# Performance work log

Measured on AMD Instinct MI355X. Metric: run time of the kernel, lower is better.

## Reference

```python
import jax, jax.numpy as jnp
from jax import lax
import numpy as np

B, C, H, W = 16, 64, 256, 256
K = 7


def setup_inputs() -> dict:
    key = jax.random.key(0)
    kx, kk = jax.random.split(key)
    x = jax.random.normal(kx, (B, C, H, W), dtype=jnp.float32)
    kernel = jax.random.normal(kk, (K, K), dtype=jnp.float32)
    return {"x": x, "kernel": kernel}


def reference(x, kernel):
    # Depthwise conv: every (b, ch) slice convolved with the SAME [K,K] kernel.
    # scipy-style true convolution => flip the kernel, 'same' padding.
    c = x.shape[1]
    kflip = jnp.flip(kernel, axis=(0, 1))
    w = jnp.tile(kflip[None, None], (c, 1, 1, 1))  # [C,1,K,K]
    y = lax.conv_general_dilated(
        x, w,
        window_strides=(1, 1),
        padding='SAME',
        feature_group_count=c,
        dimension_numbers=('NCHW', 'OIHW', 'NCHW'),
    )
    # mish(y) = y * tanh(softplus(y))
    return y * jnp.tanh(jax.nn.softplus(y))
```

## Files before the change

kernel.cpp:

```cpp
#include <hip/hip_runtime.h>


#define HW 256
#define PITCH 88
#define LROWS 70
#define NSTG 1400
#define TPB 8

typedef _Float16 f16x8 __attribute__((ext_vector_type(8)));
typedef float    f32x4 __attribute__((ext_vector_type(4)));
typedef __fp16   h2    __attribute__((ext_vector_type(2)));
union U32H2 { unsigned u; h2 h; };
union BFU   { uint4 u; f16x8 h; };

__device__ __forceinline__ float mish_f(float y) {
    float t = __expf(y);
    float u = 1.0f + t;
    float d = __fmaf_rn(u, u, 1.0f);
    return y * (1.0f - __fdividef(2.0f, d));
}

__global__ __launch_bounds__(256)
__attribute__((amdgpu_waves_per_eu(3, 5)))
void dwconv7_mish_mfma3(const float* __restrict__ x,
                        const float* __restrict__ kern,
                        float* __restrict__ out) {
    __shared__ __align__(16) _Float16 lds_in[2][LROWS * PITCH];
    __shared__ __align__(16) unsigned lds_B[7 * 256];

    const int tid = threadIdx.x;
    const int bid = blockIdx.x;
    const int plane = bid >> 1;
    const int sbase = (bid & 1) << 3;

    const float* __restrict__ xp = x + (size_t)plane * (HW * HW);
    float* __restrict__ op = out + (size_t)plane * (HW * HW);

    float kf[49];
    #pragma unroll
    for (int i = 0; i < 49; ++i) {
        int p = i / 7, q = i - p * 7;
        kf[i] = __int_as_float(__builtin_amdgcn_readfirstlane(
                    __float_as_int(kern[(6 - p) * 7 + (6 - q)])));
    }

    {
        const int j  = tid >> 4;
        const int kw = tid & 15;
        #pragma unroll
        for (int p = 0; p < 7; ++p) {
            const int d0 = 2 * kw - j - 5;
            const int d1 = d0 + 1;
            float v0 = 0.f, v1 = 0.f;
            #pragma unroll
            for (int q = 0; q < 7; ++q) {
                v0 = (d0 == q) ? kf[p * 7 + q] : v0;
                v1 = (d1 == q) ? kf[p * 7 + q] : v1;
            }
            U32H2 u; u.h = __builtin_amdgcn_cvt_pkrtz(v0, v1);
            lds_B[p * 256 + tid] = u.u;
        }
    }

    int ro_[6], co_[6], lo_[6];
    #pragma unroll
    for (int it = 0; it < 6; ++it) {
        int idx = tid + it * 256;
        int r = idx / 20, g = idx - 20 * r;
        ro_[it] = r - 3;
        co_[it] = 4 * g - 8;
        lo_[it] = r * 22 + g;
    }

    {
        const int c0 = (sbase & 3) << 6, r0 = (sbase >> 2) << 6;
        #pragma unroll
        for (int it = 0; it < 6; ++it) {
            if (it < 5 || tid < NSTG - 1280) {
                int gr = r0 + ro_[it], gc = c0 + co_[it];
                float4 f = make_float4(0.f, 0.f, 0.f, 0.f);
                if ((unsigned)gr < (unsigned)HW && (unsigned)gc <= (unsigned)(HW - 4))
                    f = *(const float4*)(xp + (gr << 8) + gc);
                U32H2 a, b;
                a.h = __builtin_amdgcn_cvt_pkrtz(f.x, f.y);
                b.h = __builtin_amdgcn_cvt_pkrtz(f.z, f.w);
                ((uint2*)lds_in[0])[lo_[it]] = make_uint2(a.u, b.u);
            }
        }
    }
    __syncthreads();

    const int lane = tid & 63;
    const int w    = tid >> 6;
    const int lrow = lane & 15;
    const int lk   = lane >> 4;

    f16x8 bfrag[7];
    #pragma unroll
    for (int p = 0; p < 7; ++p) {
        BFU bu;
        bu.u = ((const uint4*)lds_B)[p * 64 + lrow * 4 + lk];
        bfrag[p] = bu.h;
    }

    float4 rf[6];

    #pragma unroll 1
    for (int t = 0; t < TPB; ++t) {
        const int s  = sbase + t;
        const int c0 = (s & 3) << 6, r0 = (s >> 2) << 6;

        if (t + 1 < TPB) {
            const int s2 = sbase + t + 1;
            const int c2 = (s2 & 3) << 6, r2 = (s2 >> 2) << 6;
            #pragma unroll
            for (int it = 0; it < 6; ++it) {
                if (it < 5 || tid < NSTG - 1280) {
                    int gr = r2 + ro_[it], gc = c2 + co_[it];
                    rf[it] = make_float4(0.f, 0.f, 0.f, 0.f);
                    if ((unsigned)gr < (unsigned)HW && (unsigned)gc <= (unsigned)(HW - 4))
                        rf[it] = *(const float4*)(xp + (gr << 8) + gc);
                }
            }
        }
        __builtin_amdgcn_sched_barrier(0);

        const _Float16* bufp = lds_in[t & 1];
        #pragma unroll
        for (int t4 = 0; t4 < 4; ++t4) {
            f32x4 acc = {0.f, 0.f, 0.f, 0.f};
            #pragma unroll
            for (int p = 0; p < 7; ++p) {
                f16x8 a = *(const f16x8*)(bufp +
                            (16 * w + lrow + p) * PITCH + 16 * t4 + 8 * lk);
                acc = __builtin_amdgcn_mfma_f32_16x16x32_f16(a, bfrag[p], acc,
                                                             0, 0, 0);
            }
            const int col   = c0 + 16 * t4 + lrow;
            const int rbase = r0 + 16 * w + 4 * lk;
            op[(rbase + 0) * HW + col] = mish_f(acc[0]);
            op[(rbase + 1) * HW + col] = mish_f(acc[1]);
            op[(rbase + 2) * HW + col] = mish_f(acc[2]);
            op[(rbase + 3) * HW + col] = mish_f(acc[3]);
        }
        __builtin_amdgcn_sched_barrier(0);

        if (t + 1 < TPB) {
            #pragma unroll
            for (int it = 0; it < 6; ++it) {
                if (it < 5 || tid < NSTG - 1280) {
                    U32H2 a, b;
                    a.h = __builtin_amdgcn_cvt_pkrtz(rf[it].x, rf[it].y);
                    b.h = __builtin_amdgcn_cvt_pkrtz(rf[it].z, rf[it].w);
                    ((uint2*)lds_in[(t + 1) & 1])[lo_[it]] = make_uint2(a.u, b.u);
                }
            }
        }
        __syncthreads();
    }
}

extern "C" void kernel_launch(void* const* d_in, const int* in_sizes, int n_in,
                              void* d_out, int out_size, void* d_ws, size_t ws_size,
                              hipStream_t stream) {
    const float* x = (const float*)d_in[0];
    const float* k = (const float*)d_in[1];
    float* out = (float*)d_out;

    dim3 grid(2 * 16 * 64, 1, 1);
    dim3 block(256);
    dwconv7_mish_mfma3<<<grid, block, 0, stream>>>(x, k, out);
}
```

Baseline: 132.6 us.

## Give each wavefront a private double-buffered halo tile to drop block barriers

Work moves from a block-shared 64x64 tile with a 70-row LDS halo to one in which each wavefront owns a 16x64 strip with its own 22-row double-buffered LDS region. A wave loads, converts and computes its own data, so the per-tile __syncthreads is removed and waves run independently. In exchange, the halo rows loaded per output row rise from about 70/64 to 22/16, which adds redundant global loads, and LDS per block grows. The waves_per_eu upper bound is also tightened.

```diff
diff --git a/kernel.cpp b/kernel.cpp
--- a/kernel.cpp
+++ b/kernel.cpp
@@ -3,9 +3,8 @@
 
 #define HW 256
 #define PITCH 88
-#define LROWS 70
-#define NSTG 1400
-#define TPB 8
+#define WROWS 22
+#define TPW 8
 
 typedef _Float16 f16x8 __attribute__((ext_vector_type(8)));
 typedef float    f32x4 __attribute__((ext_vector_type(4)));
@@ -21,17 +20,19 @@
 }
 
 __global__ __launch_bounds__(256)
-__attribute__((amdgpu_waves_per_eu(3, 5)))
-void dwconv7_mish_mfma3(const float* __restrict__ x,
+__attribute__((amdgpu_waves_per_eu(3, 4)))
+void dwconv7_mish_mfma4(const float* __restrict__ x,
                         const float* __restrict__ kern,
                         float* __restrict__ out) {
-    __shared__ __align__(16) _Float16 lds_in[2][LROWS * PITCH];
+    __shared__ __align__(16) _Float16 lds_in[4][2][WROWS * PITCH];
     __shared__ __align__(16) unsigned lds_B[7 * 256];
 
-    const int tid = threadIdx.x;
-    const int bid = blockIdx.x;
-    const int plane = bid >> 1;
-    const int sbase = (bid & 1) << 3;
+    const int tid  = threadIdx.x;
+    const int lane = tid & 63;
+    const int w    = tid >> 6;
+    const int gw   = (blockIdx.x << 2) + w;
+    const int plane = gw >> 3;
+    const int ws    = gw & 7;
 
     const float* __restrict__ xp = x + (size_t)plane * (HW * HW);
     float* __restrict__ op = out + (size_t)plane * (HW * HW);
@@ -61,11 +62,23 @@
             lds_B[p * 256 + tid] = u.u;
         }
     }
+    __syncthreads();
 
-    int ro_[6], co_[6], lo_[6];
+    const int lrow = lane & 15;
+    const int lk   = lane >> 4;
+
+    f16x8 bfrag[7];
     #pragma unroll
-    for (int it = 0; it < 6; ++it) {
-        int idx = tid + it * 256;
+    for (int p = 0; p < 7; ++p) {
+        BFU bu;
+        bu.u = ((const uint4*)lds_B)[(p << 6) + (lrow << 2) + lk];
+        bfrag[p] = bu.h;
+    }
+
+    int ro_[7], co_[7], lo_[7];
+    #pragma unroll
+    for (int it = 0; it < 7; ++it) {
+        int idx = lane + (it << 6);
         int r = idx / 20, g = idx - 20 * r;
         ro_[it] = r - 3;
         co_[it] = 4 * g - 8;
@@ -73,49 +86,35 @@
     }
 
     {
-        const int c0 = (sbase & 3) << 6, r0 = (sbase >> 2) << 6;
+        const int r0 = ws << 5;
         #pragma unroll
-        for (int it = 0; it < 6; ++it) {
-            if (it < 5 || tid < NSTG - 1280) {
-                int gr = r0 + ro_[it], gc = c0 + co_[it];
+        for (int it = 0; it < 7; ++it) {
+            if (it < 6 || lane < 56) {
+                int gr = r0 + ro_[it], gc = co_[it];
                 float4 f = make_float4(0.f, 0.f, 0.f, 0.f);
                 if ((unsigned)gr < (unsigned)HW && (unsigned)gc <= (unsigned)(HW - 4))
                     f = *(const float4*)(xp + (gr << 8) + gc);
                 U32H2 a, b;
                 a.h = __builtin_amdgcn_cvt_pkrtz(f.x, f.y);
                 b.h = __builtin_amdgcn_cvt_pkrtz(f.z, f.w);
-                ((uint2*)lds_in[0])[lo_[it]] = make_uint2(a.u, b.u);
+                ((uint2*)lds_in[w][0])[lo_[it]] = make_uint2(a.u, b.u);
             }
         }
     }
-    __syncthreads();
 
-    const int lane = tid & 63;
-    const int w    = tid >> 6;
-    const int lrow = lane & 15;
-    const int lk   = lane >> 4;
-
-    f16x8 bfrag[7];
-    #pragma unroll
-    for (int p = 0; p < 7; ++p) {
-        BFU bu;
-        bu.u = ((const uint4*)lds_B)[p * 64 + lrow * 4 + lk];
-        bfrag[p] = bu.h;
-    }
-
-    float4 rf[6];
+    float4 rf[7];
 
     #pragma unroll 1
-    for (int t = 0; t < TPB; ++t) {
-        const int s  = sbase + t;
-        const int c0 = (s & 3) << 6, r0 = (s >> 2) << 6;
+    for (int t = 0; t < TPW; ++t) {
+        const int r0 = ((ws << 1) + (t >> 2)) << 4;
+        const int c0 = (t & 3) << 6;
 
-        if (t + 1 < TPB) {
-            const int s2 = sbase + t + 1;
-            const int c2 = (s2 & 3) << 6, r2 = (s2 >> 2) << 6;
+        if (t + 1 < TPW) {
+            const int r2 = ((ws << 1) + ((t + 1) >> 2)) << 4;
+            const int c2 = ((t + 1) & 3) << 6;
             #pragma unroll
-            for (int it = 0; it < 6; ++it) {
-                if (it < 5 || tid < NSTG - 1280) {
+            for (int it = 0; it < 7; ++it) {
+                if (it < 6 || lane < 56) {
                     int gr = r2 + ro_[it], gc = c2 + co_[it];
                     rf[it] = make_float4(0.f, 0.f, 0.f, 0.f);
                     if ((unsigned)gr < (unsigned)HW && (unsigned)gc <= (unsigned)(HW - 4))
@@ -125,38 +124,38 @@
         }
         __builtin_amdgcn_sched_barrier(0);
 
-        const _Float16* bufp = lds_in[t & 1];
+        const _Float16* bufp = lds_in[w][t & 1];
         #pragma unroll
         for (int t4 = 0; t4 < 4; ++t4) {
             f32x4 acc = {0.f, 0.f, 0.f, 0.f};
             #pragma unroll
             for (int p = 0; p < 7; ++p) {
                 f16x8 a = *(const f16x8*)(bufp +
-                            (16 * w + lrow + p) * PITCH + 16 * t4 + 8 * lk);
+                            (lrow + p) * PITCH + 16 * t4 + 8 * lk);
                 acc = __builtin_amdgcn_mfma_f32_16x16x32_f16(a, bfrag[p], acc,
                                                              0, 0, 0);
             }
-            const int col   = c0 + 16 * t4 + lrow;
-            const int rbase = r0 + 16 * w + 4 * lk;
-            op[(rbase + 0) * HW + col] = mish_f(acc[0]);
-            op[(rbase + 1) * HW + col] = mish_f(acc[1]);
-            op[(rbase + 2) * HW + col] = mish_f(acc[2]);
-            op[(rbase + 3) * HW + col] = mish_f(acc[3]);
+            const int col = c0 + 16 * t4 + lrow;
+            const int rb  = r0 + (lk << 2);
+            op[(rb + 0) * HW + col] = mish_f(acc[0]);
+            op[(rb + 1) * HW + col] = mish_f(acc[1]);
+            op[(rb + 2) * HW + col] = mish_f(acc[2]);
+            op[(rb + 3) * HW + col] = mish_f(acc[3]);
         }
         __builtin_amdgcn_sched_barrier(0);
 
-        if (t + 1 < TPB) {
+        if (t + 1 < TPW) {
+            _Float16* dstb = lds_in[w][(t + 1) & 1];
             #pragma unroll
-            for (int it = 0; it < 6; ++it) {
-                if (it < 5 || tid < NSTG - 1280) {
+            for (int it = 0; it < 7; ++it) {
+                if (it < 6 || lane < 56) {
                     U32H2 a, b;
                     a.h = __builtin_amdgcn_cvt_pkrtz(rf[it].x, rf[it].y);
                     b.h = __builtin_amdgcn_cvt_pkrtz(rf[it].z, rf[it].w);
-                    ((uint2*)lds_in[(t + 1) & 1])[lo_[it]] = make_uint2(a.u, b.u);
+                    ((uint2*)dstb)[lo_[it]] = make_uint2(a.u, b.u);
                 }
             }
         }
-        __syncthreads();
     }
 }
 
@@ -167,7 +166,7 @@
     const float* k = (const float*)d_in[1];
     float* out = (float*)d_out;
 
-    dim3 grid(2 * 16 * 64, 1, 1);
+    dim3 grid(2048, 1, 1);
     dim3 block(256);
-    dwconv7_mish_mfma3<<<grid, block, 0, stream>>>(x, k, out);
+    dwconv7_mish_mfma4<<<grid, block, 0, stream>>>(x, k, out);
 }
```

Result: slower. 155.6 us (+17.3%).
